# Kernel optimization log

Hardware: AMD Instinct MI355X
Metric: run time of the kernel (lower is better)

Reference implementation:

```python
import jax, jax.numpy as jnp
import numpy as np

ALPHA = 3.0   # config.model.hgnn_alpha
K = 16        # config.model.k_neighbors
S, N, E, D = 3, 8192, 1024, 512


def setup_inputs() -> dict:
    key = jax.random.key(0)
    k1, k2, k3 = jax.random.split(key, 3)
    x = jax.random.normal(k1, (1,), dtype=jnp.float32)  # only used for device in torch
    node_embed = jax.random.normal(k2, (S, N, D), dtype=jnp.float32)  # embednod tables
    edge_embed = jax.random.normal(k3, (S, E, D), dtype=jnp.float32)  # embedhy tables
    return {"x": x, "node_embed": node_embed, "edge_embed": edge_embed}


def reference(x, node_embed, edge_embed):
    # sim[s] = n_embed @ h_embed.T  -> [S, N, E]
    sim = jnp.einsum('snd,sed->sne', node_embed, edge_embed)
    # adj = softmax(relu(alpha * sim), dim=1 over hyperedges)
    adj = jax.nn.softmax(jax.nn.relu(ALPHA * sim), axis=-1)
    # top-k mask along hyperedge axis (scatter 1s at top-k indices per row)
    _, topk_idx = jax.lax.top_k(adj, K)  # [S, N, K]
    s_idx = jnp.arange(S)[:, None, None]
    n_idx = jnp.arange(N)[None, :, None]
    mask = jnp.zeros_like(adj).at[s_idx, n_idx, topk_idx].set(1.0)
    adj = adj * mask
    # hard threshold: binary incidence matrix per scale.
    # Original then drops all-zero hyperedge columns and returns nonzero
    # (node_idx, hyperedge_idx) pairs -- data-dependent shapes, so the dense
    # binary incidence [S, N, E] is the jit-compatible equivalent output;
    # the index lists are exactly its nonzero coordinates.
    hard = jnp.where(adj > 0.5, 1.0, 0.0)
    return hard
```

## Files before the change

### kernel.cpp

```cpp
#include <hip/hip_runtime.h>
#include <cmath>

#define SS 3
#define NN 8192
#define EE 1024
#define DD 512
#define ALPHA 3.0f
#define TAU 0.03f

typedef __attribute__((ext_vector_type(8))) short bf16x8;
typedef __attribute__((ext_vector_type(4))) float f32x4;

#define AS1(p) ((const __attribute__((address_space(1))) void*)(p))
#define AS3(p) ((__attribute__((address_space(3))) void*)(p))

__device__ __forceinline__ unsigned short f2bf(float x) {
    unsigned u = __float_as_uint(x);
    return (unsigned short)((u + 0x7fffu + ((u >> 16) & 1u)) >> 16);
}
__device__ __forceinline__ float bf2f(unsigned short h) {
    return __uint_as_float(((unsigned)h) << 16);
}

__device__ __forceinline__ void gload_lds16(const unsigned short* g, unsigned short* l) {
    __builtin_amdgcn_global_load_lds(AS1(g), AS3(l), 16, 0, 0);
}

__global__ __launch_bounds__(256)
void split_both_kernel(const float* __restrict__ node, const float* __restrict__ edge,
                       unsigned short* __restrict__ Ah, unsigned short* __restrict__ Al,
                       unsigned short* __restrict__ Bh, unsigned short* __restrict__ Bl)
{
    const int nA = SS * NN * DD / 4;
    const int nB = SS * EE * DD / 4;
    int i = blockIdx.x * blockDim.x + threadIdx.x;

    const float4* src;
    unsigned short* hi;
    unsigned short* lo;
    int idx;
    if (i < nA) {
        src = (const float4*)node; hi = Ah; lo = Al; idx = i;
    } else if (i < nA + nB) {
        src = (const float4*)edge; hi = Bh; lo = Bl; idx = i - nA;
    } else {
        return;
    }
    float4 v = src[idx];
    ushort4 h, l;
    h.x = f2bf(v.x); l.x = f2bf(v.x - bf2f(h.x));
    h.y = f2bf(v.y); l.y = f2bf(v.y - bf2f(h.y));
    h.z = f2bf(v.z); l.z = f2bf(v.z - bf2f(h.z));
    h.w = f2bf(v.w); l.w = f2bf(v.w - bf2f(h.w));
    ((ushort4*)hi)[idx] = h;
    ((ushort4*)lo)[idx] = l;
}

__global__ __launch_bounds__(512, 2)
void gemm_mfma_kernel(const unsigned short* __restrict__ Ah,
                      const unsigned short* __restrict__ Al,
                      const unsigned short* __restrict__ Bh,
                      const unsigned short* __restrict__ Bl,
                      float* __restrict__ out)
{
    const int s  = blockIdx.z;
    const int m0 = blockIdx.x * 256;
    const int n0 = blockIdx.y * 256;

    const unsigned short* pAh = Ah + (size_t)s * NN * DD;
    const unsigned short* pAl = Al + (size_t)s * NN * DD;
    const unsigned short* pBh = Bh + (size_t)s * EE * DD;
    const unsigned short* pBl = Bl + (size_t)s * EE * DD;
    float* C = out + (size_t)s * NN * EE;

    __shared__ unsigned short lds[2 * 512 * 64];

    const int t    = threadIdx.x;
    const int lane = t & 63;
    const int wid  = t >> 6;
    const int wm   = wid >> 2;
    const int wn   = wid & 3;
    const int fr   = lane & 15;
    const int kg   = lane >> 4;

    f32x4 acc[8][4];
#pragma unroll
    for (int i = 0; i < 8; ++i)
#pragma unroll
        for (int j = 0; j < 4; ++j) acc[i][j] = (f32x4){0.f, 0.f, 0.f, 0.f};

    auto stage = [&](int buf, int k0) {
#pragma unroll
        for (int i = 0; i < 8; ++i) {
            const int c    = i * 512 + t;
            const int row  = c >> 3;
            const int slot = c & 7;
            const int j    = slot ^ (row & 7);
            const unsigned short* src;
            if (row < 256) {
                src = (j < 4) ? pAh + (size_t)(m0 + row) * DD + k0 + j * 8
                              : pAl + (size_t)(m0 + row) * DD + k0 + (j - 4) * 8;
            } else {
                const int rn = row - 256;
                src = (j < 4) ? pBh + (size_t)(n0 + rn) * DD + k0 + j * 8
                              : pBl + (size_t)(n0 + rn) * DD + k0 + (j - 4) * 8;
            }
            gload_lds16(src, &lds[buf * 32768 + c * 8]);
        }
    };

    auto compute = [&](int buf) {
        const unsigned short* L = &lds[buf * 32768];
        bf16x8 bh[4], bl[4];
#pragma unroll
        for (int j = 0; j < 4; ++j) {
            const int r = 256 + wn * 64 + j * 16 + fr;
            bh[j] = *(const bf16x8*)&L[r * 64 + ((kg)     ^ (r & 7)) * 8];
            bl[j] = *(const bf16x8*)&L[r * 64 + ((4 + kg) ^ (r & 7)) * 8];
        }
        __builtin_amdgcn_s_setprio(1);
#pragma unroll
        for (int i = 0; i < 8; ++i) {
            const int r = wm * 128 + i * 16 + fr;
            bf16x8 ah = *(const bf16x8*)&L[r * 64 + ((kg)     ^ (r & 7)) * 8];
            bf16x8 al = *(const bf16x8*)&L[r * 64 + ((4 + kg) ^ (r & 7)) * 8];
#pragma unroll
            for (int j = 0; j < 4; ++j) {
                acc[i][j] = __builtin_amdgcn_mfma_f32_16x16x32_bf16(ah, bh[j], acc[i][j], 0, 0, 0);
                acc[i][j] = __builtin_amdgcn_mfma_f32_16x16x32_bf16(ah, bl[j], acc[i][j], 0, 0, 0);
                acc[i][j] = __builtin_amdgcn_mfma_f32_16x16x32_bf16(al, bh[j], acc[i][j], 0, 0, 0);
            }
        }
        __builtin_amdgcn_s_setprio(0);
    };

    stage(0, 0);
    __syncthreads();

#pragma unroll 1
    for (int ks = 0; ks < 15; ++ks) {
        stage((ks + 1) & 1, (ks + 1) * 32);
        compute(ks & 1);
        __syncthreads();
    }
    compute(15 & 1);

#pragma unroll
    for (int i = 0; i < 8; ++i)
#pragma unroll
        for (int j = 0; j < 4; ++j) {
            const int col = n0 + wn * 64 + j * 16 + fr;
#pragma unroll
            for (int r = 0; r < 4; ++r) {
                const int row = m0 + wm * 128 + i * 16 + kg * 4 + r;
                C[(size_t)row * EE + col] = fmaxf(ALPHA * acc[i][j][r], 0.f);
            }
        }
}

__global__ void zero_count_kernel(int* __restrict__ count) {
    if (threadIdx.x == 0 && blockIdx.x == 0) count[0] = 0;
}

__global__ __launch_bounds__(256)
void softmax_threshold_flag_kernel(float* __restrict__ out,
                                   int* __restrict__ count,
                                   int* __restrict__ worklist)
{
    const int wave = threadIdx.x >> 6;
    const int lane = threadIdx.x & 63;
    const size_t row = (size_t)blockIdx.x * 4 + wave;
    float* p = out + row * EE;

    float z[16];
    float m = 0.f;
#pragma unroll
    for (int j = 0; j < 4; ++j) {
        float4 v = *(const float4*)(p + j * 256 + lane * 4);
        z[j*4+0] = v.x; z[j*4+1] = v.y; z[j*4+2] = v.z; z[j*4+3] = v.w;
        m = fmaxf(m, fmaxf(fmaxf(v.x, v.y), fmaxf(v.z, v.w)));
    }
#pragma unroll
    for (int off = 32; off >= 1; off >>= 1)
        m = fmaxf(m, __shfl_xor(m, off, 64));

    float e[16];
    float sum = 0.f;
#pragma unroll
    for (int j = 0; j < 16; ++j) {
        e[j] = expf(z[j] - m);
        sum += e[j];
    }
#pragma unroll
    for (int off = 32; off >= 1; off >>= 1)
        sum += __shfl_xor(sum, off, 64);

    const float thr = 0.5f * sum;
    const float T   = m + logf(thr);
    int lf = 0;
#pragma unroll
    for (int j = 0; j < 16; ++j)
        lf |= (fabsf(z[j] - T) < TAU) ? 1 : 0;

#pragma unroll
    for (int j = 0; j < 4; ++j) {
        float4 o;
        o.x = (e[j*4+0] > thr) ? 1.f : 0.f;
        o.y = (e[j*4+1] > thr) ? 1.f : 0.f;
        o.z = (e[j*4+2] > thr) ? 1.f : 0.f;
        o.w = (e[j*4+3] > thr) ? 1.f : 0.f;
        *(float4*)(p + j * 256 + lane * 4) = o;
    }
    const int anyf = __any(lf);
    if (anyf && lane == 0) {
        int idx = atomicAdd(count, 1);
        worklist[idx] = (int)row;
    }
}

__global__ __launch_bounds__(256)
void fixup_z_kernel(const float* __restrict__ node, const float* __restrict__ edge,
                    const int* __restrict__ count, const int* __restrict__ worklist,
                    float* __restrict__ zbuf, int zcap)
{
    __shared__ float sa[DD];
    const int t    = threadIdx.x;
    const int lane = t & 63;
    const int wid  = t >> 6;

    int nwork = count[0];
    if (nwork > zcap) nwork = zcap;
    const int items = nwork * 4;

    for (int item = blockIdx.x; item < items; item += gridDim.x) {
        const int w   = item >> 2;
        const int row = worklist[w];
        const int c0  = (item & 3) * 256;
        const int s   = row / NN;
        const float* a = node + (size_t)row * DD;
        const float* B = edge + (size_t)s * EE * DD;

        __syncthreads();
        if (t < DD / 4) ((float4*)sa)[t] = ((const float4*)a)[t];
        __syncthreads();

        const float4 va0 = ((const float4*)sa)[lane];
        const float4 va1 = ((const float4*)sa)[64 + lane];

        const int cbase = c0 + wid * 64;
        for (int g = 0; g < 16; ++g) {
            float acc[4];
#pragma unroll
            for (int j = 0; j < 4; ++j) {
                const float* b = B + (size_t)(cbase + g * 4 + j) * DD;
                float4 b0 = *(const float4*)(b + lane * 4);
                float4 b1 = *(const float4*)(b + 256 + lane * 4);
                float av;
                av = va0.x * b0.x;
                av = fmaf(va0.y, b0.y, av);
                av = fmaf(va0.z, b0.z, av);
                av = fmaf(va0.w, b0.w, av);
                av = fmaf(va1.x, b1.x, av);
                av = fmaf(va1.y, b1.y, av);
                av = fmaf(va1.z, b1.z, av);
                av = fmaf(va1.w, b1.w, av);
                acc[j] = av;
            }
#pragma unroll
            for (int off = 32; off >= 1; off >>= 1) {
#pragma unroll
                for (int j = 0; j < 4; ++j)
                    acc[j] += __shfl_xor(acc[j], off, 64);
            }
            if (lane == 0) {
#pragma unroll
                for (int j = 0; j < 4; ++j)
                    zbuf[(size_t)w * EE + cbase + g * 4 + j] = fmaxf(ALPHA * acc[j], 0.f);
            }
        }
    }
}

__global__ __launch_bounds__(256)
void fixup_finish_kernel(const float* __restrict__ zbuf,
                         const int* __restrict__ count, const int* __restrict__ worklist,
                         float* __restrict__ out, int zcap)
{
    const int lane = threadIdx.x & 63;
    const int wid  = threadIdx.x >> 6;
    int nwork = count[0];
    if (nwork > zcap) nwork = zcap;

    for (int w = blockIdx.x * 4 + wid; w < nwork; w += gridDim.x * 4) {
        const int row = worklist[w];
        const float* p = zbuf + (size_t)w * EE;

        float z[16];
        float m = 0.f;
#pragma unroll
        for (int j = 0; j < 4; ++j) {
            float4 v = *(const float4*)(p + j * 256 + lane * 4);
            z[j*4+0] = v.x; z[j*4+1] = v.y; z[j*4+2] = v.z; z[j*4+3] = v.w;
            m = fmaxf(m, fmaxf(fmaxf(v.x, v.y), fmaxf(v.z, v.w)));
        }
#pragma unroll
        for (int off = 32; off >= 1; off >>= 1)
            m = fmaxf(m, __shfl_xor(m, off, 64));

        float e[16], sum = 0.f;
#pragma unroll
        for (int j = 0; j < 16; ++j) { e[j] = expf(z[j] - m); sum += e[j]; }
#pragma unroll
        for (int off = 32; off >= 1; off >>= 1)
            sum += __shfl_xor(sum, off, 64);

        const float thr = 0.5f * sum;
        float* q = out + (size_t)row * EE;
#pragma unroll
        for (int j = 0; j < 4; ++j) {
            float4 o;
            o.x = (e[j*4+0] > thr) ? 1.f : 0.f;
            o.y = (e[j*4+1] > thr) ? 1.f : 0.f;
            o.z = (e[j*4+2] > thr) ? 1.f : 0.f;
            o.w = (e[j*4+3] > thr) ? 1.f : 0.f;
            *(float4*)(q + j * 256 + lane * 4) = o;
        }
    }
}

__global__ __launch_bounds__(256)
void fixup2_kernel(const float* __restrict__ node, const float* __restrict__ edge,
                   const int* __restrict__ count, const int* __restrict__ worklist,
                   float* __restrict__ out, int start)
{
    __shared__ float sa[DD];
    __shared__ float zrow[EE];
    __shared__ float red[8];

    const int t    = threadIdx.x;
    const int lane = t & 63;
    const int wid  = t >> 6;
    const int nwork = count[0];

    for (int w = start + blockIdx.x; w < nwork; w += gridDim.x) {
        const int row = worklist[w];
        const int s = row / NN;
        const float* a = node + (size_t)row * DD;
        const float* B = edge + (size_t)s * EE * DD;

        __syncthreads();
        if (t < DD / 4) ((float4*)sa)[t] = ((const float4*)a)[t];
        __syncthreads();

        float4 va0 = ((const float4*)sa)[lane];
        float4 va1 = ((const float4*)sa)[64 + lane];

        for (int c = wid; c < EE; c += 4) {
            const float* b = B + (size_t)c * DD;
            float4 b0 = *(const float4*)(b + lane * 4);
            float4 b1 = *(const float4*)(b + 256 + lane * 4);
            float acc;
            acc = va0.x * b0.x;
            acc = fmaf(va0.y, b0.y, acc);
            acc = fmaf(va0.z, b0.z, acc);
            acc = fmaf(va0.w, b0.w, acc);
            acc = fmaf(va1.x, b1.x, acc);
            acc = fmaf(va1.y, b1.y, acc);
            acc = fmaf(va1.z, b1.z, acc);
            acc = fmaf(va1.w, b1.w, acc);
#pragma unroll
            for (int off = 32; off >= 1; off >>= 1)
                acc += __shfl_xor(acc, off, 64);
            if (lane == 0) zrow[c] = fmaxf(ALPHA * acc, 0.f);
        }
        __syncthreads();

        float z[4], m = 0.f;
#pragma unroll
        for (int j = 0; j < 4; ++j) {
            z[j] = zrow[j * 256 + t];
            m = fmaxf(m, z[j]);
        }
#pragma unroll
        for (int off = 32; off >= 1; off >>= 1)
            m = fmaxf(m, __shfl_xor(m, off, 64));
        if (lane == 0) red[wid] = m;
        __syncthreads();
        m = fmaxf(fmaxf(red[0], red[1]), fmaxf(red[2], red[3]));

        float e[4], sum = 0.f;
#pragma unroll
        for (int j = 0; j < 4; ++j) { e[j] = expf(z[j] - m); sum += e[j]; }
#pragma unroll
        for (int off = 32; off >= 1; off >>= 1)
            sum += __shfl_xor(sum, off, 64);
        if (lane == 0) red[4 + wid] = sum;
        __syncthreads();
        sum = red[4] + red[5] + red[6] + red[7];

        const float thr = 0.5f * sum;
#pragma unroll
        for (int j = 0; j < 4; ++j)
            out[(size_t)row * EE + j * 256 + t] = (e[j] > thr) ? 1.f : 0.f;
        __syncthreads();
    }
}

#define BM 128
#define BN 128
#define BK 16
#define TM 8
#define TN 8

__global__ __launch_bounds__(256, 2)
void gemm_relu_kernel(const float* __restrict__ node,
                      const float* __restrict__ edge,
                      float* __restrict__ out)
{
    const int s  = blockIdx.z;
    const int m0 = blockIdx.y * BM;
    const int n0 = blockIdx.x * BN;

    const float* A = node + (size_t)s * NN * DD;
    const float* B = edge + (size_t)s * EE * DD;
    float*       C = out  + (size_t)s * NN * EE;

    __shared__ float As[BK][BM + 4];
    __shared__ float Bs[BK][BN + 4];

    const int tid = threadIdx.x;
    const int tx  = tid % 16;
    const int ty  = tid / 16;
    const int lrow = tid / 4;
    const int lcol = (tid % 4) * 4;

    float acc[TM][TN];
#pragma unroll
    for (int i = 0; i < TM; ++i)
#pragma unroll
        for (int j = 0; j < TN; ++j) acc[i][j] = 0.f;

    for (int k0 = 0; k0 < DD; k0 += BK) {
#pragma unroll
        for (int p = 0; p < 2; ++p) {
            const int r = lrow + p * 64;
            float4 v = *(const float4*)(A + (size_t)(m0 + r) * DD + k0 + lcol);
            As[lcol + 0][r] = v.x; As[lcol + 1][r] = v.y;
            As[lcol + 2][r] = v.z; As[lcol + 3][r] = v.w;
            float4 w = *(const float4*)(B + (size_t)(n0 + r) * DD + k0 + lcol);
            Bs[lcol + 0][r] = w.x; Bs[lcol + 1][r] = w.y;
            Bs[lcol + 2][r] = w.z; Bs[lcol + 3][r] = w.w;
        }
        __syncthreads();
#pragma unroll
        for (int k = 0; k < BK; ++k) {
            float a[TM], b[TN];
            float4 a0 = *(const float4*)&As[k][ty * 8];
            float4 a1 = *(const float4*)&As[k][ty * 8 + 4];
            a[0]=a0.x; a[1]=a0.y; a[2]=a0.z; a[3]=a0.w;
            a[4]=a1.x; a[5]=a1.y; a[6]=a1.z; a[7]=a1.w;
            float4 b0 = *(const float4*)&Bs[k][tx * 8];
            float4 b1 = *(const float4*)&Bs[k][tx * 8 + 4];
            b[0]=b0.x; b[1]=b0.y; b[2]=b0.z; b[3]=b0.w;
            b[4]=b1.x; b[5]=b1.y; b[6]=b1.z; b[7]=b1.w;
#pragma unroll
            for (int i = 0; i < TM; ++i)
#pragma unroll
                for (int j = 0; j < TN; ++j)
                    acc[i][j] = fmaf(a[i], b[j], acc[i][j]);
        }
        __syncthreads();
    }
#pragma unroll
    for (int i = 0; i < TM; ++i) {
        const size_t row = (size_t)(m0 + ty * 8 + i);
        float4 o0, o1;
        o0.x = fmaxf(ALPHA * acc[i][0], 0.f);
        o0.y = fmaxf(ALPHA * acc[i][1], 0.f);
        o0.z = fmaxf(ALPHA * acc[i][2], 0.f);
        o0.w = fmaxf(ALPHA * acc[i][3], 0.f);
        o1.x = fmaxf(ALPHA * acc[i][4], 0.f);
        o1.y = fmaxf(ALPHA * acc[i][5], 0.f);
        o1.z = fmaxf(ALPHA * acc[i][6], 0.f);
        o1.w = fmaxf(ALPHA * acc[i][7], 0.f);
        *(float4*)(C + row * EE + n0 + tx * 8)     = o0;
        *(float4*)(C + row * EE + n0 + tx * 8 + 4) = o1;
    }
}

__global__ __launch_bounds__(256)
void softmax_threshold_kernel(float* __restrict__ out)
{
    const int wave = threadIdx.x >> 6;
    const int lane = threadIdx.x & 63;
    const size_t row = (size_t)blockIdx.x * 4 + wave;
    float* p = out + row * EE;

    float z[16];
    float m = 0.f;
#pragma unroll
    for (int j = 0; j < 4; ++j) {
        float4 v = *(const float4*)(p + j * 256 + lane * 4);
        z[j*4+0] = v.x; z[j*4+1] = v.y; z[j*4+2] = v.z; z[j*4+3] = v.w;
        m = fmaxf(m, fmaxf(fmaxf(v.x, v.y), fmaxf(v.z, v.w)));
    }
#pragma unroll
    for (int off = 32; off >= 1; off >>= 1)
        m = fmaxf(m, __shfl_xor(m, off, 64));
    float e[16], sum = 0.f;
#pragma unroll
    for (int j = 0; j < 16; ++j) { e[j] = expf(z[j] - m); sum += e[j]; }
#pragma unroll
    for (int off = 32; off >= 1; off >>= 1)
        sum += __shfl_xor(sum, off, 64);
    const float thr = 0.5f * sum;
#pragma unroll
    for (int j = 0; j < 4; ++j) {
        float4 o;
        o.x = (e[j*4+0] > thr) ? 1.f : 0.f;
        o.y = (e[j*4+1] > thr) ? 1.f : 0.f;
        o.z = (e[j*4+2] > thr) ? 1.f : 0.f;
        o.w = (e[j*4+3] > thr) ? 1.f : 0.f;
        *(float4*)(p + j * 256 + lane * 4) = o;
    }
}

extern "C" void kernel_launch(void* const* d_in, const int* in_sizes, int n_in,
                              void* d_out, int out_size, void* d_ws, size_t ws_size,
                              hipStream_t stream) {
    const float* node = (const float*)d_in[1];
    const float* edge = (const float*)d_in[2];
    float* out = (float*)d_out;

    const size_t SAe = (size_t)SS * NN * DD;
    const size_t SBe = (size_t)SS * EE * DD;
    const size_t split_bytes = (2 * SAe + 2 * SBe) * 2;
    const size_t wl_bytes    = (size_t)(SS * NN + 1) * 4;
    const size_t base_need   = split_bytes + wl_bytes;

    if (ws_size >= base_need) {
        unsigned short* Ah = (unsigned short*)d_ws;
        unsigned short* Al = Ah + SAe;
        unsigned short* Bh = Al + SAe;
        unsigned short* Bl = Bh + SBe;
        int* count    = (int*)(Bl + SBe);
        int* worklist = count + 1;

        const size_t zoff = (base_need + 255) & ~(size_t)255;
        int zcap = 0;
        if (ws_size > zoff) {
            size_t zc = (ws_size - zoff) / ((size_t)EE * 4);
            zcap = (int)(zc > 4096 ? 4096 : zc);
        }
        float* zbuf = (float*)((char*)d_ws + zoff);

        const int n4 = (int)((SAe + SBe) / 4);
        split_both_kernel<<<(n4 + 255) / 256, 256, 0, stream>>>(node, edge, Ah, Al, Bh, Bl);

        zero_count_kernel<<<1, 64, 0, stream>>>(count);

        dim3 g1(NN / 256, EE / 256, SS);
        gemm_mfma_kernel<<<g1, 512, 0, stream>>>(Ah, Al, Bh, Bl, out);

        softmax_threshold_flag_kernel<<<(SS * NN) / 4, 256, 0, stream>>>(out, count, worklist);

        if (zcap > 0) {
            fixup_z_kernel<<<1024, 256, 0, stream>>>(node, edge, count, worklist, zbuf, zcap);
            fixup_finish_kernel<<<64, 256, 0, stream>>>(zbuf, count, worklist, out, zcap);
        }
        fixup2_kernel<<<512, 256, 0, stream>>>(node, edge, count, worklist, out, zcap);
    } else {
        dim3 g1(EE / BN, NN / BM, SS);
        gemm_relu_kernel<<<g1, 256, 0, stream>>>(node, edge, out);
        softmax_threshold_kernel<<<(SS * NN) / 4, 256, 0, stream>>>(out);
    }
}
```

Before: 153.9 us.

## Restructure split-bf16 GEMM to 128x256 tiles with 32x32 MFMA and split-K pipelining

Rewrites the three-pass bf16 GEMM main loop. Tiles shrink from 256x256 to 128x256, so twice as many blocks launch. The kernel moves from 16x16x32 to 32x32x16 MFMA instructions. Each 32-wide K step is split into two half-phases that issue the next tile's global-to-LDS loads before computing, synchronized with explicit vmcnt waits and raw barriers. The aim is more occupancy and latency hiding and fewer LDS reads per MFMA. The cost is more global traffic from the smaller M tile and fragile hand-written waitcnt logic. The last iteration also prefetches a wrapped-around tile it never uses.

Measured after the change: 284.8 us. +85.0%, slower.

```diff
diff --git a/kernel.cpp b/kernel.cpp
--- a/kernel.cpp
+++ b/kernel.cpp
@@ -10,6 +10,7 @@
 
 typedef __attribute__((ext_vector_type(8))) short bf16x8;
 typedef __attribute__((ext_vector_type(4))) float f32x4;
+typedef __attribute__((ext_vector_type(16))) float f32x16;
 
 #define AS1(p) ((const __attribute__((address_space(1))) void*)(p))
 #define AS3(p) ((__attribute__((address_space(3))) void*)(p))
@@ -64,7 +65,7 @@
                       float* __restrict__ out)
 {
     const int s  = blockIdx.z;
-    const int m0 = blockIdx.x * 256;
+    const int m0 = blockIdx.x * 128;
     const int n0 = blockIdx.y * 256;
 
     const unsigned short* pAh = Ah + (size_t)s * NN * DD;
@@ -73,87 +74,100 @@
     const unsigned short* pBl = Bl + (size_t)s * EE * DD;
     float* C = out + (size_t)s * NN * EE;
 
-    __shared__ unsigned short lds[2 * 512 * 64];
+    __shared__ unsigned short lds[2 * 24576];
 
     const int t    = threadIdx.x;
     const int lane = t & 63;
     const int wid  = t >> 6;
     const int wm   = wid >> 2;
     const int wn   = wid & 3;
-    const int fr   = lane & 15;
-    const int kg   = lane >> 4;
-
-    f32x4 acc[8][4];
-#pragma unroll
-    for (int i = 0; i < 8; ++i)
-#pragma unroll
-        for (int j = 0; j < 4; ++j) acc[i][j] = (f32x4){0.f, 0.f, 0.f, 0.f};
-
-    auto stage = [&](int buf, int k0) {
-#pragma unroll
-        for (int i = 0; i < 8; ++i) {
-            const int c    = i * 512 + t;
-            const int row  = c >> 3;
-            const int slot = c & 7;
-            const int j    = slot ^ (row & 7);
+    const int fr   = lane & 31;
+    const int kp   = lane >> 5;
+
+    f32x16 acc[2][2];
+#pragma unroll
+    for (int p = 0; p < 2; ++p)
+#pragma unroll
+        for (int nf = 0; nf < 2; ++nf)
+#pragma unroll
+            for (int r = 0; r < 16; ++r) acc[p][nf][r] = 0.f;
+
+    auto issue_kh = [&](int kh, int buf, int k0) {
+#pragma unroll
+        for (int i = 0; i < 3; ++i) {
+            const int span = wid * 3 + i;
+            const int pl   = span / 12;
+            const int sp   = span % 12;
+            const int r    = sp * 32 + (lane >> 1);
+            const size_t goff = (size_t)k0 + kh * 16 + (lane & 1) * 8;
             const unsigned short* src;
-            if (row < 256) {
-                src = (j < 4) ? pAh + (size_t)(m0 + row) * DD + k0 + j * 8
-                              : pAl + (size_t)(m0 + row) * DD + k0 + (j - 4) * 8;
+            if (sp < 4) {
+                src = (pl ? pAl : pAh) + (size_t)(m0 + r) * DD + goff;
             } else {
-                const int rn = row - 256;
-                src = (j < 4) ? pBh + (size_t)(n0 + rn) * DD + k0 + j * 8
-                              : pBl + (size_t)(n0 + rn) * DD + k0 + (j - 4) * 8;
-            }
-            gload_lds16(src, &lds[buf * 32768 + c * 8]);
+                src = (pl ? pBl : pBh) + (size_t)(n0 + r - 128) * DD + goff;
+            }
+            gload_lds16(src, &lds[buf * 24576 + (pl * 2 + kh) * 6144 + sp * 512 + lane * 8]);
         }
     };
 
-    auto compute = [&](int buf) {
-        const unsigned short* L = &lds[buf * 32768];
-        bf16x8 bh[4], bl[4];
-#pragma unroll
-        for (int j = 0; j < 4; ++j) {
-            const int r = 256 + wn * 64 + j * 16 + fr;
-            bh[j] = *(const bf16x8*)&L[r * 64 + ((kg)     ^ (r & 7)) * 8];
-            bl[j] = *(const bf16x8*)&L[r * 64 + ((4 + kg) ^ (r & 7)) * 8];
-        }
+    auto phase = [&](int kh, int buf, int nbuf, int kn) {
+        bf16x8 a[2][2], b[2][2];
+#pragma unroll
+        for (int p = 0; p < 2; ++p)
+#pragma unroll
+            for (int pl = 0; pl < 2; ++pl) {
+                const int row = wm * 64 + p * 32 + fr;
+                a[p][pl] = *(const bf16x8*)&lds[buf * 24576 + (pl * 2 + kh) * 6144 + row * 16 + kp * 8];
+            }
+#pragma unroll
+        for (int nf = 0; nf < 2; ++nf)
+#pragma unroll
+            for (int pl = 0; pl < 2; ++pl) {
+                const int row = 128 + wn * 64 + nf * 32 + fr;
+                b[nf][pl] = *(const bf16x8*)&lds[buf * 24576 + (pl * 2 + kh) * 6144 + row * 16 + kp * 8];
+            }
+
+        issue_kh(kh, nbuf, kn);
+
+        asm volatile("s_waitcnt vmcnt(3)" ::: "memory");
+        __builtin_amdgcn_s_barrier();
+
         __builtin_amdgcn_s_setprio(1);
 #pragma unroll
-        for (int i = 0; i < 8; ++i) {
-            const int r = wm * 128 + i * 16 + fr;
-            bf16x8 ah = *(const bf16x8*)&L[r * 64 + ((kg)     ^ (r & 7)) * 8];
-            bf16x8 al = *(const bf16x8*)&L[r * 64 + ((4 + kg) ^ (r & 7)) * 8];
-#pragma unroll
-            for (int j = 0; j < 4; ++j) {
-                acc[i][j] = __builtin_amdgcn_mfma_f32_16x16x32_bf16(ah, bh[j], acc[i][j], 0, 0, 0);
-                acc[i][j] = __builtin_amdgcn_mfma_f32_16x16x32_bf16(ah, bl[j], acc[i][j], 0, 0, 0);
-                acc[i][j] = __builtin_amdgcn_mfma_f32_16x16x32_bf16(al, bh[j], acc[i][j], 0, 0, 0);
-            }
+        for (int p = 0; p < 2; ++p) {
+            acc[p][0] = __builtin_amdgcn_mfma_f32_32x32x16_bf16(a[p][0], b[0][0], acc[p][0], 0, 0, 0);
+            acc[p][1] = __builtin_amdgcn_mfma_f32_32x32x16_bf16(a[p][0], b[1][0], acc[p][1], 0, 0, 0);
+            acc[p][0] = __builtin_amdgcn_mfma_f32_32x32x16_bf16(a[p][0], b[0][1], acc[p][0], 0, 0, 0);
+            acc[p][1] = __builtin_amdgcn_mfma_f32_32x32x16_bf16(a[p][0], b[1][1], acc[p][1], 0, 0, 0);
+            acc[p][0] = __builtin_amdgcn_mfma_f32_32x32x16_bf16(a[p][1], b[0][0], acc[p][0], 0, 0, 0);
+            acc[p][1] = __builtin_amdgcn_mfma_f32_32x32x16_bf16(a[p][1], b[1][0], acc[p][1], 0, 0, 0);
         }
         __builtin_amdgcn_s_setprio(0);
     };
 
-    stage(0, 0);
-    __syncthreads();
+    issue_kh(0, 0, 0);
+    issue_kh(1, 0, 0);
+    asm volatile("s_waitcnt vmcnt(3)" ::: "memory");
+    __builtin_amdgcn_s_barrier();
 
 #pragma unroll 1
-    for (int ks = 0; ks < 15; ++ks) {
-        stage((ks + 1) & 1, (ks + 1) * 32);
-        compute(ks & 1);
-        __syncthreads();
-    }
-    compute(15 & 1);
-
-#pragma unroll
-    for (int i = 0; i < 8; ++i)
-#pragma unroll
-        for (int j = 0; j < 4; ++j) {
-            const int col = n0 + wn * 64 + j * 16 + fr;
-#pragma unroll
-            for (int r = 0; r < 4; ++r) {
-                const int row = m0 + wm * 128 + i * 16 + kg * 4 + r;
-                C[(size_t)row * EE + col] = fmaxf(ALPHA * acc[i][j][r], 0.f);
+    for (int ks = 0; ks < 16; ++ks) {
+        const int buf  = ks & 1;
+        const int nbuf = buf ^ 1;
+        const int kn   = ((ks + 1) & 15) * 32;
+        phase(0, buf, nbuf, kn);
+        phase(1, buf, nbuf, kn);
+    }
+
+#pragma unroll
+    for (int p = 0; p < 2; ++p)
+#pragma unroll
+        for (int nf = 0; nf < 2; ++nf) {
+            const int col = n0 + wn * 64 + nf * 32 + fr;
+#pragma unroll
+            for (int r = 0; r < 16; ++r) {
+                const int row = m0 + wm * 64 + p * 32 + (r & 3) + 8 * (r >> 2) + 4 * kp;
+                C[(size_t)row * EE + col] = fmaxf(ALPHA * acc[p][nf][r], 0.f);
             }
         }
 }
@@ -559,7 +573,7 @@
 
         zero_count_kernel<<<1, 64, 0, stream>>>(count);
 
-        dim3 g1(NN / 256, EE / 256, SS);
+        dim3 g1(NN / 128, EE / 256, SS);
         gemm_mfma_kernel<<<g1, 512, 0, stream>>>(Ah, Al, Bh, Bl, out);
 
         softmax_threshold_flag_kernel<<<(SS * NN) / 4, 256, 0, stream>>>(out, count, worklist);
```
